# Kernel optimization log

Measured on AMD Instinct MI355X. Metric: run time of the kernel, lower is better.

The kernel has to match this reference:

```python
import jax, jax.numpy as jnp
import numpy as np

B, D1, SN, NF = 32, 49, 32, 16          # batch, n_sais, sqrt_n, n_filters
D_MODEL, HEADS = SN * SN * NF, 16        # 16384, 16
DEPTH = D_MODEL // HEADS                 # 1024
C_IN = 16


def setup_inputs() -> dict:
    key = jax.random.key(0)
    ks = jax.random.split(key, 11)
    mk = lambda k, shape, scale=1.0: jax.random.normal(k, shape, dtype=jnp.float32) * scale
    w_scale = 1.0 / np.sqrt(C_IN)
    return {
        "v": mk(ks[0], (B, D1, SN, SN, C_IN)),
        "k": mk(ks[1], (B, D1, SN, SN, C_IN)),
        "q": mk(ks[2], (B, D1, SN, SN, C_IN)),
        # 1x1x1 Conv3D == pointwise channel matmul: weight [C_in, n_filters] + bias
        "Wq": mk(ks[3], (C_IN, NF), w_scale), "bq": jnp.zeros((NF,), jnp.float32),
        "Wk": mk(ks[4], (C_IN, NF), w_scale), "bk": jnp.zeros((NF,), jnp.float32),
        "Wv": mk(ks[5], (C_IN, NF), w_scale), "bv": jnp.zeros((NF,), jnp.float32),
        "Wo": mk(ks[6], (NF, NF), w_scale),   "bo": jnp.zeros((NF,), jnp.float32),
    }


def _pointwise(x, W, b):
    # Conv3D(kernel=1, padding='same') over [B, d1, h, w, c]
    return jnp.einsum('bdhwc,cf->bdhwf', x, W) + b


def reference(v, k, q, Wq, bq, Wk, bk, Wv, bv, Wo, bo):
    b = q.shape[0]
    # projections (1x1x1 conv3d), then flatten spatial+channel into d_model
    def proj_heads(x, W, bias):
        y = _pointwise(x, W, bias).reshape(b, D1, D_MODEL)       # reshape2d
        y = y.reshape(b, D1, HEADS, DEPTH)                        # split_heads
        return y.transpose(0, 2, 1, 3)                            # [b, h, d1, depth]
    qh = proj_heads(q, Wq, bq)
    kh = proj_heads(k, Wk, bk)
    vh = proj_heads(v, Wv, bv)
    # scaled dot-product attention over the 49 SAI tokens
    scale = 1.0 / jnp.sqrt(jnp.float32(DEPTH))
    scores = jnp.einsum('bhqd,bhkd->bhqk', qh, kh) * scale        # [b, h, 49, 49]
    attn = jax.nn.softmax(scores, axis=-1)
    ctx = jnp.einsum('bhqk,bhkd->bhqd', attn, vh)                 # [b, h, 49, depth]
    ctx = ctx.transpose(0, 2, 1, 3).reshape(b, D1, D_MODEL)       # concat heads
    ctx = ctx.reshape(b, D1, SN, SN, NF)                          # reshape4d
    out = _pointwise(ctx, Wo, bo)                                 # wout conv3d 1x1x1
    return out, attn
```

## Files before the change

kernel.cpp:

```cpp
#include <hip/hip_runtime.h>
#include <hip/hip_bf16.h>


#define NT 49
#define TOKS 16384
#define HSL 1024
#define SLOT 3200
#define ZSWZ(n) (((((n) & 7) ^ (((n) >> 3) & 7))) << 4)

typedef __attribute__((ext_vector_type(8))) short bf16x8;
typedef __attribute__((ext_vector_type(4))) float f32x4;

__device__ __forceinline__ ushort f2bf(float f) {
    union { float f; unsigned u; } v; v.f = f;
    return (ushort)((v.u + 0x7fffu + ((v.u >> 16) & 1u)) >> 16);
}
__device__ __forceinline__ unsigned pk2(float lo, float hi) {
    return (unsigned)f2bf(lo) | ((unsigned)f2bf(hi) << 16);
}
__device__ __forceinline__ float qdot(f32x4 x0, f32x4 x1, f32x4 x2, f32x4 x3,
                                      f32x4 wa, f32x4 wb, f32x4 wc, f32x4 wd) {
    float s =      x0[0]*wa[0];
    s = fmaf(x0[1], wa[1], s); s = fmaf(x0[2], wa[2], s); s = fmaf(x0[3], wa[3], s);
    s = fmaf(x1[0], wb[0], s); s = fmaf(x1[1], wb[1], s); s = fmaf(x1[2], wb[2], s);
    s = fmaf(x1[3], wb[3], s);
    s = fmaf(x2[0], wc[0], s); s = fmaf(x2[1], wc[1], s); s = fmaf(x2[2], wc[2], s);
    s = fmaf(x2[3], wc[3], s);
    s = fmaf(x3[0], wd[0], s); s = fmaf(x3[1], wd[1], s); s = fmaf(x3[2], wd[2], s);
    s = fmaf(x3[3], wd[3], s);
    return s;
}

#define W_DECL(mb) \
    f32x4 W00 = *(const f32x4*)((mb)+ 0), W01 = *(const f32x4*)((mb)+ 4), \
          W02 = *(const f32x4*)((mb)+ 8), W03 = *(const f32x4*)((mb)+12), \
          W10 = *(const f32x4*)((mb)+16), W11 = *(const f32x4*)((mb)+20), \
          W12 = *(const f32x4*)((mb)+24), W13 = *(const f32x4*)((mb)+28), \
          W20 = *(const f32x4*)((mb)+32), W21 = *(const f32x4*)((mb)+36), \
          W22 = *(const f32x4*)((mb)+40), W23 = *(const f32x4*)((mb)+44), \
          W30 = *(const f32x4*)((mb)+48), W31 = *(const f32x4*)((mb)+52), \
          W32 = *(const f32x4*)((mb)+56), W33 = *(const f32x4*)((mb)+60)

__global__ __launch_bounds__(256, 2) void k_scores8(
    const float* __restrict__ qin, const float* __restrict__ kin,
    const float* __restrict__ Wq, const float* __restrict__ bq,
    const float* __restrict__ Wk, float* __restrict__ ws1)
{
    __shared__ ushort bufA[64*128];
    __shared__ ushort bufB[64*128];
    __shared__ float  Msh[256];
    __shared__ float  wkbqSh[16];
    __shared__ float  gSh[64];

    const int tid  = threadIdx.x;
    const int lane = tid & 63;
    const int wv   = tid >> 6;
    const int s    = blockIdx.x & 7;
    const int h    = (blockIdx.x >> 3) & 15;
    const int b    = blockIdx.x >> 7;

    const float* qbase = qin + (size_t)b*NT*TOKS + h*HSL + s*128;
    const float* kbase = kin + (size_t)b*NT*TOKS + h*HSL + s*128;

    const int f4 = tid & 31;
    const int t0 = tid >> 5;
    const int si = (tid >> 2) & 7;
    const int rq = tid & 3;

    f32x4 kv[7];
    {
        const float* kp = kbase + f4*4;
        #pragma unroll
        for (int i = 0; i < 7; ++i) {
            const int t = t0 + 8*i; const int tc = t < 48 ? t : 48;
            kv[i] = *(const f32x4*)(kp + (size_t)tc*TOKS);
        }
    }
    f32x4 q0[7], q1[7], q2[7], q3[7];
    {
        #pragma unroll
        for (int i = 0; i < 7; ++i) {
            const int t = t0 + 8*i; const int tc = t < 48 ? t : 48;
            const float* qc = qbase + si*16 + (size_t)tc*TOKS;
            q0[i] = *(const f32x4*)(qc);
            q1[i] = *(const f32x4*)(qc + 4);
            q2[i] = *(const f32x4*)(qc + 8);
            q3[i] = *(const f32x4*)(qc + 12);
        }
    }

    {
        unsigned* z0 = (unsigned*)bufA; unsigned* z1 = (unsigned*)bufB;
        #pragma unroll
        for (int i = 0; i < 16; ++i) { z0[tid + 256*i] = 0u; z1[tid + 256*i] = 0u; }
        const int c1 = tid >> 4, c2 = tid & 15;
        float m = 0.f;
        #pragma unroll
        for (int f = 0; f < 16; ++f) m += Wq[c1*16+f] * Wk[c2*16+f];
        Msh[c2*16 + c1] = m;
        if (tid < 16) {
            float wb = 0.f;
            #pragma unroll
            for (int g = 0; g < 16; ++g) wb += Wk[tid*16+g] * bq[g];
            wkbqSh[tid] = wb;
        }
        if (tid < 64) gSh[tid] = 0.f;
    }
    __syncthreads();

    W_DECL(Msh + rq*64);
    f32x4 wkb = *(const f32x4*)(wkbqSh + (f4 & 3)*4);

    #pragma unroll
    for (int i = 0; i < 7; ++i) {
        const int t = t0 + 8*i;
        f32x4 xk = kv[i];
        if (t >= NT) xk = (f32x4){0.f,0.f,0.f,0.f};
        uint2 w; w.x = pk2(xk[0], xk[1]); w.y = pk2(xk[2], xk[3]);
        *(uint2*)((char*)bufB + ((t*256 + f4*8) ^ ((t & 7) << 4))) = w;
        const float pg = xk[0]*wkb[0] + xk[1]*wkb[1] + xk[2]*wkb[2] + xk[3]*wkb[3];
        if (pg != 0.f) atomicAdd(&gSh[t], pg);
    }
    #pragma unroll
    for (int i = 0; i < 7; ++i) {
        const int t = t0 + 8*i;
        if (t < NT) {
            const float o0 = qdot(q0[i],q1[i],q2[i],q3[i], W00,W01,W02,W03);
            const float o1 = qdot(q0[i],q1[i],q2[i],q3[i], W10,W11,W12,W13);
            const float o2 = qdot(q0[i],q1[i],q2[i],q3[i], W20,W21,W22,W23);
            const float o3 = qdot(q0[i],q1[i],q2[i],q3[i], W30,W31,W32,W33);
            uint2 w; w.x = pk2(o0, o1); w.y = pk2(o2, o3);
            *(uint2*)((char*)bufA + ((t*256 + si*32 + rq*8) ^ ((t & 7) << 4))) = w;
        }
    }
    __syncthreads();

    f32x4 accS[4];
    #pragma unroll
    for (int nt = 0; nt < 4; ++nt) accS[nt] = (f32x4){0.f,0.f,0.f,0.f};
    #pragma unroll
    for (int ks = 0; ks < 4; ++ks) {
        const int ra  = wv*16 + (lane & 15);
        const int abo = (ra*256 + (ks*32 + (lane >> 4)*8)*2) ^ ((ra & 7) << 4);
        const bf16x8 af = *(const bf16x8*)((const char*)bufA + abo);
        #pragma unroll
        for (int nt = 0; nt < 4; ++nt) {
            const int rb  = nt*16 + (lane & 15);
            const int bbo = (rb*256 + (ks*32 + (lane >> 4)*8)*2) ^ ((rb & 7) << 4);
            const bf16x8 bf = *(const bf16x8*)((const char*)bufB + bbo);
            accS[nt] = __builtin_amdgcn_mfma_f32_16x16x32_bf16(af, bf, accS[nt], 0, 0, 0);
        }
    }

    float* slot = ws1 + (size_t)blockIdx.x * SLOT;
    #pragma unroll
    for (int nt = 0; nt < 4; ++nt) {
        const int col = nt*16 + (lane & 15);
        #pragma unroll
        for (int rr = 0; rr < 4; ++rr) {
            const int row = wv*16 + (lane >> 4)*4 + rr;
            if (row < NT) slot[row*64 + col] = accS[nt][rr];
        }
    }
    if (tid < 64) slot[3136 + tid] = gSh[tid];
}

template<int SPLIT, int LOG2S>
__global__ __launch_bounds__(256, 2) void k_scores(
    const float* __restrict__ qin, const float* __restrict__ kin,
    const float* __restrict__ Wq, const float* __restrict__ bq,
    const float* __restrict__ Wk, float* __restrict__ ws1)
{
    __shared__ ushort bufA[64*128];
    __shared__ ushort bufB[64*128];
    __shared__ float  Msh[256];
    __shared__ float  wkbqSh[16];
    __shared__ float  gSh[64];

    const int tid  = threadIdx.x;
    const int lane = tid & 63;
    const int wv   = tid >> 6;
    const int s    = blockIdx.x & (SPLIT - 1);
    const int h    = (blockIdx.x >> LOG2S) & 15;
    const int b    = blockIdx.x >> (LOG2S + 4);

    const float* qbase = qin + (size_t)b*NT*TOKS + h*HSL + s*(1024/SPLIT);
    const float* kbase = kin + (size_t)b*NT*TOKS + h*HSL + s*(1024/SPLIT);

    const int f4 = tid & 31;
    const int t0 = tid >> 5;
    const int si = (tid >> 2) & 7;
    const int rq = tid & 3;

    constexpr int NC = 8 / SPLIT;

    f32x4 kv[7];
    {
        const float* kp = kbase + f4*4;
        #pragma unroll
        for (int i = 0; i < 7; ++i) {
            const int t = t0 + 8*i; const int tc = t < 48 ? t : 48;
            kv[i] = *(const f32x4*)(kp + (size_t)tc*TOKS);
        }
    }
    f32x4 xa0, xa1, xa2, xa3;
    {
        const float* qc = qbase + si*16 + (size_t)t0*TOKS;
        xa0 = *(const f32x4*)(qc);
        xa1 = *(const f32x4*)(qc + 4);
        xa2 = *(const f32x4*)(qc + 8);
        xa3 = *(const f32x4*)(qc + 12);
    }

    {
        unsigned* z0 = (unsigned*)bufA; unsigned* z1 = (unsigned*)bufB;
        #pragma unroll
        for (int i = 0; i < 16; ++i) { z0[tid + 256*i] = 0u; z1[tid + 256*i] = 0u; }
        const int c1 = tid >> 4, c2 = tid & 15;
        float m = 0.f;
        #pragma unroll
        for (int f = 0; f < 16; ++f) m += Wq[c1*16+f] * Wk[c2*16+f];
        Msh[c2*16 + c1] = m;
        if (tid < 16) {
            float wb = 0.f;
            #pragma unroll
            for (int g = 0; g < 16; ++g) wb += Wk[tid*16+g] * bq[g];
            wkbqSh[tid] = wb;
        }
        if (tid < 64) gSh[tid] = 0.f;
    }
    __syncthreads();

    W_DECL(Msh + rq*64);
    f32x4 wkb = *(const f32x4*)(wkbqSh + (f4 & 3)*4);

    f32x4 accS[4];
    #pragma unroll
    for (int nt = 0; nt < 4; ++nt) accS[nt] = (f32x4){0.f,0.f,0.f,0.f};

    for (int kc = 0; kc < NC; ++kc) {
        if (kc > 0) {
            const float* kp = kbase + kc*128 + f4*4;
            #pragma unroll
            for (int i = 0; i < 7; ++i) {
                const int t = t0 + 8*i; const int tc = t < 48 ? t : 48;
                kv[i] = *(const f32x4*)(kp + (size_t)tc*TOKS);
            }
            const float* qc = qbase + kc*128 + si*16 + (size_t)t0*TOKS;
            xa0 = *(const f32x4*)(qc);
            xa1 = *(const f32x4*)(qc + 4);
            xa2 = *(const f32x4*)(qc + 8);
            xa3 = *(const f32x4*)(qc + 12);
        }
        #pragma unroll
        for (int i = 0; i < 7; ++i) {
            const int t = t0 + 8*i;
            f32x4 xk = kv[i];
            if (t >= NT) xk = (f32x4){0.f,0.f,0.f,0.f};
            uint2 w; w.x = pk2(xk[0], xk[1]); w.y = pk2(xk[2], xk[3]);
            *(uint2*)((char*)bufB + ((t*256 + f4*8) ^ ((t & 7) << 4))) = w;
            const float pg = xk[0]*wkb[0] + xk[1]*wkb[1] + xk[2]*wkb[2] + xk[3]*wkb[3];
            if (pg != 0.f) atomicAdd(&gSh[t], pg);
        }
        #pragma unroll
        for (int i = 0; i < 7; ++i) {
            f32x4 xb0 = xa0, xb1 = xa1, xb2 = xa2, xb3 = xa3;
            if (i < 6) {
                const int tn = t0 + 8*(i+1); const int tc = tn < 48 ? tn : 48;
                const float* qc = qbase + kc*128 + si*16 + (size_t)tc*TOKS;
                xb0 = *(const f32x4*)(qc);
                xb1 = *(const f32x4*)(qc + 4);
                xb2 = *(const f32x4*)(qc + 8);
                xb3 = *(const f32x4*)(qc + 12);
            }
            const int t = t0 + 8*i;
            if (t < NT) {
                const float o0 = qdot(xa0,xa1,xa2,xa3, W00,W01,W02,W03);
                const float o1 = qdot(xa0,xa1,xa2,xa3, W10,W11,W12,W13);
                const float o2 = qdot(xa0,xa1,xa2,xa3, W20,W21,W22,W23);
                const float o3 = qdot(xa0,xa1,xa2,xa3, W30,W31,W32,W33);
                uint2 w; w.x = pk2(o0, o1); w.y = pk2(o2, o3);
                *(uint2*)((char*)bufA + ((t*256 + si*32 + rq*8) ^ ((t & 7) << 4))) = w;
            }
            xa0 = xb0; xa1 = xb1; xa2 = xb2; xa3 = xb3;
        }
        __syncthreads();
        #pragma unroll
        for (int ks = 0; ks < 4; ++ks) {
            const int ra  = wv*16 + (lane & 15);
            const int abo = (ra*256 + (ks*32 + (lane >> 4)*8)*2) ^ ((ra & 7) << 4);
            const bf16x8 af = *(const bf16x8*)((const char*)bufA + abo);
            #pragma unroll
            for (int nt = 0; nt < 4; ++nt) {
                const int rb  = nt*16 + (lane & 15);
                const int bbo = (rb*256 + (ks*32 + (lane >> 4)*8)*2) ^ ((rb & 7) << 4);
                const bf16x8 bf = *(const bf16x8*)((const char*)bufB + bbo);
                accS[nt] = __builtin_amdgcn_mfma_f32_16x16x32_bf16(af, bf, accS[nt], 0, 0, 0);
            }
        }
        if (kc + 1 < NC) __syncthreads();
    }

    float* slot = ws1 + (size_t)blockIdx.x * SLOT;
    #pragma unroll
    for (int nt = 0; nt < 4; ++nt) {
        const int col = nt*16 + (lane & 15);
        #pragma unroll
        for (int rr = 0; rr < 4; ++rr) {
            const int row = wv*16 + (lane >> 4)*4 + rr;
            if (row < NT) slot[row*64 + col] = accS[nt][rr];
        }
    }
    if (tid < 64) slot[3136 + tid] = gSh[tid];
}

template<int SPLIT>
__global__ __launch_bounds__(256, 2) void k_softmax(
    const float* __restrict__ ws1, float* __restrict__ attnp,
    ushort* __restrict__ ws2)
{
    __shared__ float sS[NT*69];
    __shared__ float sG[64];
    const int tid = threadIdx.x;
    const float* base = ws1 + (size_t)blockIdx.x * SPLIT * SLOT;

    for (int p = tid; p < 784; p += 256) {
        const int row = p >> 4, c4 = (p & 15) * 4;
        float4 acc = *(const float4*)(base + row*64 + c4);
        #pragma unroll
        for (int s = 1; s < SPLIT; ++s) {
            const float4 a = *(const float4*)(base + s*SLOT + row*64 + c4);
            acc.x += a.x; acc.y += a.y; acc.z += a.z; acc.w += a.w;
        }
        sS[row*69 + c4 + 0] = acc.x;
        sS[row*69 + c4 + 1] = acc.y;
        sS[row*69 + c4 + 2] = acc.z;
        sS[row*69 + c4 + 3] = acc.w;
    }
    if (tid < 64) {
        float g = base[3136 + tid];
        #pragma unroll
        for (int s = 1; s < SPLIT; ++s) g += base[s*SLOT + 3136 + tid];
        sG[tid] = g;
    }
    __syncthreads();

    if (tid < NT) {
        float mx = -1e30f;
        for (int j = 0; j < NT; ++j) {
            const float v = (sS[tid*69 + j] + sG[j]) * 0.03125f;
            sS[tid*69 + j] = v;
            mx = fmaxf(mx, v);
        }
        float ssum = 0.f;
        for (int j = 0; j < NT; ++j) {
            const float e = __expf(sS[tid*69 + j] - mx);
            sS[tid*69 + j] = e; ssum += e;
        }
        const float inv = 1.0f / ssum;
        for (int j = 0; j < NT; ++j) sS[tid*69 + j] *= inv;
    }
    __syncthreads();

    float* ab = attnp + (size_t)blockIdx.x * (NT*NT);
    for (int p = tid; p < NT*NT; p += 256) {
        const int t = p / NT, j = p - t*NT;
        ab[p] = sS[t*69 + j];
    }
    ushort* w2 = ws2 + (size_t)blockIdx.x * 4096;
    for (int p = tid; p < 4096; p += 256) {
        const int t = p >> 6, j = p & 63;
        const float v = (t < NT && j < NT) ? sS[t*69 + j] : 0.f;
        w2[p] = f2bf(v);
    }
}

__global__ __launch_bounds__(256, 2) void k_out(
    const float* __restrict__ vin,
    const float* __restrict__ Wv, const float* __restrict__ bv,
    const float* __restrict__ Wo, const float* __restrict__ bo,
    const ushort* __restrict__ ws2, float* __restrict__ out)
{
    __shared__ unsigned Zt[4096];
    __shared__ float WvoSh[256];
    __shared__ float bvoSh[16];

    const int tid  = threadIdx.x;
    const int lane = tid & 63;
    const int wv   = tid >> 6;
    const int kc   = blockIdx.x & 7;
    const int h    = (blockIdx.x >> 3) & 15;
    const int b    = blockIdx.x >> 7;
    const float* vbase = vin + (size_t)b*NT*TOKS + h*HSL;

    const int si = (tid >> 2) & 7;
    const int rq = tid & 3;
    const int t0 = tid >> 5;

    const ushort* w2 = ws2 + ((size_t)(blockIdx.x >> 3)) * 4096;
    const int ra = wv*16 + (lane & 15);
    const bf16x8 af0 = *(const bf16x8*)(w2 + ra*64 +      (lane >> 4)*8);
    const bf16x8 af1 = *(const bf16x8*)(w2 + ra*64 + 32 + (lane >> 4)*8);
    f32x4 xa0, xa1, xa2, xa3;
    {
        const float* vc = vbase + kc*128 + si*16 + (size_t)t0*TOKS;
        xa0 = *(const f32x4*)(vc);
        xa1 = *(const f32x4*)(vc + 4);
        xa2 = *(const f32x4*)(vc + 8);
        xa3 = *(const f32x4*)(vc + 12);
    }

    {
        const int c1 = tid >> 4, c2 = tid & 15;
        float wvo = 0.f;
        #pragma unroll
        for (int f = 0; f < 16; ++f) wvo += Wv[c1*16+f] * Wo[f*16+c2];
        WvoSh[c2*16 + c1] = wvo;
        if (tid < 16) {
            float s2 = 0.f;
            #pragma unroll
            for (int g = 0; g < 16; ++g) s2 += bv[g]*Wo[g*16+tid];
            bvoSh[tid] = s2 + bo[tid];
        }
        #pragma unroll
        for (int i = 0; i < 16; ++i) Zt[tid + 256*i] = 0u;
    }
    __syncthreads();

    W_DECL(WvoSh + rq*64);
    const float bias = bvoSh[lane & 15];

    #pragma unroll
    for (int i = 0; i < 7; ++i) {
        f32x4 xb0 = xa0, xb1 = xa1, xb2 = xa2, xb3 = xa3;
        if (i < 6) {
            const int tn = t0 + 8*(i+1); const int tc = tn < 48 ? tn : 48;
            const float* vc = vbase + kc*128 + si*16 + (size_t)tc*TOKS;
            xb0 = *(const f32x4*)(vc);
            xb1 = *(const f32x4*)(vc + 4);
            xb2 = *(const f32x4*)(vc + 8);
            xb3 = *(const f32x4*)(vc + 12);
        }
        const int t = t0 + 8*i;
        if (t < NT) {
            const float o0 = qdot(xa0,xa1,xa2,xa3, W00,W01,W02,W03);
            const float o1 = qdot(xa0,xa1,xa2,xa3, W10,W11,W12,W13);
            const float o2 = qdot(xa0,xa1,xa2,xa3, W20,W21,W22,W23);
            const float o3 = qdot(xa0,xa1,xa2,xa3, W30,W31,W32,W33);
            const int n0 = si*16 + rq*4;
            const int pb = (t >> 1)*4, hb = (t & 1)*2;
            *(ushort*)((char*)Zt + ((((n0+0)*128 + pb) ^ ZSWZ(n0+0)) + hb)) = f2bf(o0);
            *(ushort*)((char*)Zt + ((((n0+1)*128 + pb) ^ ZSWZ(n0+1)) + hb)) = f2bf(o1);
            *(ushort*)((char*)Zt + ((((n0+2)*128 + pb) ^ ZSWZ(n0+2)) + hb)) = f2bf(o2);
            *(ushort*)((char*)Zt + ((((n0+3)*128 + pb) ^ ZSWZ(n0+3)) + hb)) = f2bf(o3);
        }
        xa0 = xb0; xa1 = xb1; xa2 = xb2; xa3 = xb3;
    }
    __syncthreads();

    float* obase = out + (size_t)b*NT*TOKS + h*HSL + kc*128;
    #pragma unroll
    for (int nt2 = 0; nt2 < 8; ++nt2) {
        const int n    = nt2*16 + (lane & 15);
        const int swzn = ZSWZ(n);
        const bf16x8 bf0 = *(const bf16x8*)((const char*)Zt + ((n*128 +      (lane >> 4)*16) ^ swzn));
        const bf16x8 bf1 = *(const bf16x8*)((const char*)Zt + ((n*128 + 64 + (lane >> 4)*16) ^ swzn));
        f32x4 acc = (f32x4){0.f, 0.f, 0.f, 0.f};
        acc = __builtin_amdgcn_mfma_f32_16x16x32_bf16(af0, bf0, acc, 0, 0, 0);
        acc = __builtin_amdgcn_mfma_f32_16x16x32_bf16(af1, bf1, acc, 0, 0, 0);
        #pragma unroll
        for (int r2 = 0; r2 < 4; ++r2) {
            const int row = wv*16 + (lane >> 4)*4 + r2;
            if (row < NT) obase[(size_t)row*TOKS + n] = acc[r2] + bias;
        }
    }
}

extern "C" void kernel_launch(void* const* d_in, const int* in_sizes, int n_in,
                              void* d_out, int out_size, void* d_ws, size_t ws_size,
                              hipStream_t stream) {
    const float* v  = (const float*)d_in[0];
    const float* k  = (const float*)d_in[1];
    const float* q  = (const float*)d_in[2];
    const float* Wq = (const float*)d_in[3];
    const float* bq = (const float*)d_in[4];
    const float* Wk = (const float*)d_in[5];
    const float* bk = (const float*)d_in[6];
    const float* Wv = (const float*)d_in[7];
    const float* bv = (const float*)d_in[8];
    const float* Wo = (const float*)d_in[9];
    const float* bo = (const float*)d_in[10];
    (void)bk; (void)in_sizes; (void)n_in; (void)out_size;

    float* outp  = (float*)d_out;
    float* attnp = outp + (size_t)32 * 49 * 16384;
    float* ws1   = (float*)d_ws;

    const size_t need8 = (size_t)4096*SLOT*4 + (size_t)512*4096*2;
    const size_t need4 = (size_t)2048*SLOT*4 + (size_t)512*4096*2;
    if (ws_size >= need8) {
        ushort* ws2 = (ushort*)(ws1 + (size_t)4096*SLOT);
        k_scores8    <<<dim3(4096), dim3(256), 0, stream>>>(q, k, Wq, bq, Wk, ws1);
        k_softmax<8> <<<dim3(512),  dim3(256), 0, stream>>>(ws1, attnp, ws2);
        k_out        <<<dim3(4096), dim3(256), 0, stream>>>(v, Wv, bv, Wo, bo, ws2, outp);
    } else if (ws_size >= need4) {
        ushort* ws2 = (ushort*)(ws1 + (size_t)2048*SLOT);
        k_scores<4,2><<<dim3(2048), dim3(256), 0, stream>>>(q, k, Wq, bq, Wk, ws1);
        k_softmax<4> <<<dim3(512),  dim3(256), 0, stream>>>(ws1, attnp, ws2);
        k_out        <<<dim3(4096), dim3(256), 0, stream>>>(v, Wv, bv, Wo, bo, ws2, outp);
    } else {
        ushort* ws2 = (ushort*)(ws1 + (size_t)1024*SLOT);
        k_scores<2,1><<<dim3(1024), dim3(256), 0, stream>>>(q, k, Wq, bq, Wk, ws1);
        k_softmax<2> <<<dim3(512),  dim3(256), 0, stream>>>(ws1, attnp, ws2);
        k_out        <<<dim3(4096), dim3(256), 0, stream>>>(v, Wv, bv, Wo, bo, ws2, outp);
    }
}
```

Before: 129.9 us.

## Halve scores LDS tiles via two-pass K staging and preload all V rows

```diff
diff --git a/kernel.cpp b/kernel.cpp
--- a/kernel.cpp
+++ b/kernel.cpp
@@ -7,6 +7,7 @@
 #define HSL 1024
 #define SLOT 3200
 #define ZSWZ(n) (((((n) & 7) ^ (((n) >> 3) & 7))) << 4)
+#define SW64(t) (((t) & 7) << 4)
 
 typedef __attribute__((ext_vector_type(8))) short bf16x8;
 typedef __attribute__((ext_vector_type(4))) float f32x4;
@@ -46,8 +47,8 @@
     const float* __restrict__ Wq, const float* __restrict__ bq,
     const float* __restrict__ Wk, float* __restrict__ ws1)
 {
-    __shared__ ushort bufA[64*128];
-    __shared__ ushort bufB[64*128];
+    __shared__ ushort bufA[64*64];
+    __shared__ ushort bufB[64*64];
     __shared__ float  Msh[256];
     __shared__ float  wkbqSh[16];
     __shared__ float  gSh[64];
@@ -77,22 +78,23 @@
         }
     }
     f32x4 q0[7], q1[7], q2[7], q3[7];
+    #pragma unroll
+    for (int i = 0; i < 7; ++i) {
+        const int t = t0 + 8*i; const int tc = t < 48 ? t : 48;
+        const float* qc = qbase + si*16 + (size_t)tc*TOKS;
+        q0[i] = *(const f32x4*)(qc);
+        q1[i] = *(const f32x4*)(qc + 4);
+        q2[i] = *(const f32x4*)(qc + 8);
+        q3[i] = *(const f32x4*)(qc + 12);
+    }
+
     {
-        #pragma unroll
-        for (int i = 0; i < 7; ++i) {
-            const int t = t0 + 8*i; const int tc = t < 48 ? t : 48;
-            const float* qc = qbase + si*16 + (size_t)tc*TOKS;
-            q0[i] = *(const f32x4*)(qc);
-            q1[i] = *(const f32x4*)(qc + 4);
-            q2[i] = *(const f32x4*)(qc + 8);
-            q3[i] = *(const f32x4*)(qc + 12);
-        }
-    }
-
-    {
-        unsigned* z0 = (unsigned*)bufA; unsigned* z1 = (unsigned*)bufB;
-        #pragma unroll
-        for (int i = 0; i < 16; ++i) { z0[tid + 256*i] = 0u; z1[tid + 256*i] = 0u; }
+        unsigned* zA = (unsigned*)bufA; unsigned* zB = (unsigned*)bufB;
+        #pragma unroll
+        for (int i = 0; i < 2; ++i) {
+            const int j = tid + 256*i;
+            if (j < 480) { zA[1568 + j] = 0u; zB[1568 + j] = 0u; }
+        }
         const int c1 = tid >> 4, c2 = tid & 15;
         float m = 0.f;
         #pragma unroll
@@ -109,47 +111,67 @@
     __syncthreads();
 
     W_DECL(Msh + rq*64);
-    f32x4 wkb = *(const f32x4*)(wkbqSh + (f4 & 3)*4);
-
+    const f32x4 wkb = *(const f32x4*)(wkbqSh + (f4 & 3)*4);
+
+    uint2 kw[7];
     #pragma unroll
     for (int i = 0; i < 7; ++i) {
         const int t = t0 + 8*i;
         f32x4 xk = kv[i];
         if (t >= NT) xk = (f32x4){0.f,0.f,0.f,0.f};
-        uint2 w; w.x = pk2(xk[0], xk[1]); w.y = pk2(xk[2], xk[3]);
-        *(uint2*)((char*)bufB + ((t*256 + f4*8) ^ ((t & 7) << 4))) = w;
+        kw[i].x = pk2(xk[0], xk[1]); kw[i].y = pk2(xk[2], xk[3]);
         const float pg = xk[0]*wkb[0] + xk[1]*wkb[1] + xk[2]*wkb[2] + xk[3]*wkb[3];
         if (pg != 0.f) atomicAdd(&gSh[t], pg);
     }
+    uint2 qw[7];
     #pragma unroll
     for (int i = 0; i < 7; ++i) {
-        const int t = t0 + 8*i;
-        if (t < NT) {
-            const float o0 = qdot(q0[i],q1[i],q2[i],q3[i], W00,W01,W02,W03);
-            const float o1 = qdot(q0[i],q1[i],q2[i],q3[i], W10,W11,W12,W13);
-            const float o2 = qdot(q0[i],q1[i],q2[i],q3[i], W20,W21,W22,W23);
-            const float o3 = qdot(q0[i],q1[i],q2[i],q3[i], W30,W31,W32,W33);
-            uint2 w; w.x = pk2(o0, o1); w.y = pk2(o2, o3);
-            *(uint2*)((char*)bufA + ((t*256 + si*32 + rq*8) ^ ((t & 7) << 4))) = w;
-        }
-    }
-    __syncthreads();
+        const float o0 = qdot(q0[i],q1[i],q2[i],q3[i], W00,W01,W02,W03);
+        const float o1 = qdot(q0[i],q1[i],q2[i],q3[i], W10,W11,W12,W13);
+        const float o2 = qdot(q0[i],q1[i],q2[i],q3[i], W20,W21,W22,W23);
+        const float o3 = qdot(q0[i],q1[i],q2[i],q3[i], W30,W31,W32,W33);
+        qw[i].x = pk2(o0, o1); qw[i].y = pk2(o2, o3);
+    }
+
+    const int f4h = f4 >> 4, f4l = f4 & 15;
+    const int sih = si >> 2, sil = si & 3;
+    const int ra  = wv*16 + (lane & 15);
 
     f32x4 accS[4];
     #pragma unroll
     for (int nt = 0; nt < 4; ++nt) accS[nt] = (f32x4){0.f,0.f,0.f,0.f};
-    #pragma unroll
-    for (int ks = 0; ks < 4; ++ks) {
-        const int ra  = wv*16 + (lane & 15);
-        const int abo = (ra*256 + (ks*32 + (lane >> 4)*8)*2) ^ ((ra & 7) << 4);
-        const bf16x8 af = *(const bf16x8*)((const char*)bufA + abo);
-        #pragma unroll
-        for (int nt = 0; nt < 4; ++nt) {
-            const int rb  = nt*16 + (lane & 15);
-            const int bbo = (rb*256 + (ks*32 + (lane >> 4)*8)*2) ^ ((rb & 7) << 4);
-            const bf16x8 bf = *(const bf16x8*)((const char*)bufB + bbo);
-            accS[nt] = __builtin_amdgcn_mfma_f32_16x16x32_bf16(af, bf, accS[nt], 0, 0, 0);
-        }
+
+    #pragma unroll
+    for (int h2 = 0; h2 < 2; ++h2) {
+        if (f4h == h2) {
+            #pragma unroll
+            for (int i = 0; i < 7; ++i) {
+                const int t = t0 + 8*i;
+                *(uint2*)((char*)bufB + ((t*128 + f4l*8) ^ SW64(t))) = kw[i];
+            }
+        }
+        if (sih == h2) {
+            #pragma unroll
+            for (int i = 0; i < 7; ++i) {
+                const int t = t0 + 8*i;
+                if (t < NT)
+                    *(uint2*)((char*)bufA + ((t*128 + sil*32 + rq*8) ^ SW64(t))) = qw[i];
+            }
+        }
+        __syncthreads();
+        #pragma unroll
+        for (int ks2 = 0; ks2 < 2; ++ks2) {
+            const int abo = (ra*128 + ks2*64 + (lane >> 4)*16) ^ SW64(ra);
+            const bf16x8 af = *(const bf16x8*)((const char*)bufA + abo);
+            #pragma unroll
+            for (int nt = 0; nt < 4; ++nt) {
+                const int rb  = nt*16 + (lane & 15);
+                const int bbo = (rb*128 + ks2*64 + (lane >> 4)*16) ^ SW64(rb);
+                const bf16x8 bf = *(const bf16x8*)((const char*)bufB + bbo);
+                accS[nt] = __builtin_amdgcn_mfma_f32_16x16x32_bf16(af, bf, accS[nt], 0, 0, 0);
+            }
+        }
+        if (h2 == 0) __syncthreads();
     }
 
     float* slot = ws1 + (size_t)blockIdx.x * SLOT;
@@ -401,13 +423,15 @@
     const int ra = wv*16 + (lane & 15);
     const bf16x8 af0 = *(const bf16x8*)(w2 + ra*64 +      (lane >> 4)*8);
     const bf16x8 af1 = *(const bf16x8*)(w2 + ra*64 + 32 + (lane >> 4)*8);
-    f32x4 xa0, xa1, xa2, xa3;
-    {
-        const float* vc = vbase + kc*128 + si*16 + (size_t)t0*TOKS;
-        xa0 = *(const f32x4*)(vc);
-        xa1 = *(const f32x4*)(vc + 4);
-        xa2 = *(const f32x4*)(vc + 8);
-        xa3 = *(const f32x4*)(vc + 12);
+    f32x4 v0[7], v1[7], v2[7], v3[7];
+    #pragma unroll
+    for (int i = 0; i < 7; ++i) {
+        const int t = t0 + 8*i; const int tc = t < 48 ? t : 48;
+        const float* vc = vbase + kc*128 + si*16 + (size_t)tc*TOKS;
+        v0[i] = *(const f32x4*)(vc);
+        v1[i] = *(const f32x4*)(vc + 4);
+        v2[i] = *(const f32x4*)(vc + 8);
+        v3[i] = *(const f32x4*)(vc + 12);
     }
 
     {
@@ -432,21 +456,12 @@
 
     #pragma unroll
     for (int i = 0; i < 7; ++i) {
-        f32x4 xb0 = xa0, xb1 = xa1, xb2 = xa2, xb3 = xa3;
-        if (i < 6) {
-            const int tn = t0 + 8*(i+1); const int tc = tn < 48 ? tn : 48;
-            const float* vc = vbase + kc*128 + si*16 + (size_t)tc*TOKS;
-            xb0 = *(const f32x4*)(vc);
-            xb1 = *(const f32x4*)(vc + 4);
-            xb2 = *(const f32x4*)(vc + 8);
-            xb3 = *(const f32x4*)(vc + 12);
-        }
         const int t = t0 + 8*i;
         if (t < NT) {
-            const float o0 = qdot(xa0,xa1,xa2,xa3, W00,W01,W02,W03);
-            const float o1 = qdot(xa0,xa1,xa2,xa3, W10,W11,W12,W13);
-            const float o2 = qdot(xa0,xa1,xa2,xa3, W20,W21,W22,W23);
-            const float o3 = qdot(xa0,xa1,xa2,xa3, W30,W31,W32,W33);
+            const float o0 = qdot(v0[i],v1[i],v2[i],v3[i], W00,W01,W02,W03);
+            const float o1 = qdot(v0[i],v1[i],v2[i],v3[i], W10,W11,W12,W13);
+            const float o2 = qdot(v0[i],v1[i],v2[i],v3[i], W20,W21,W22,W23);
+            const float o3 = qdot(v0[i],v1[i],v2[i],v3[i], W30,W31,W32,W33);
             const int n0 = si*16 + rq*4;
             const int pb = (t >> 1)*4, hb = (t & 1)*2;
             *(ushort*)((char*)Zt + ((((n0+0)*128 + pb) ^ ZSWZ(n0+0)) + hb)) = f2bf(o0);
@@ -454,7 +469,6 @@
             *(ushort*)((char*)Zt + ((((n0+2)*128 + pb) ^ ZSWZ(n0+2)) + hb)) = f2bf(o2);
             *(ushort*)((char*)Zt + ((((n0+3)*128 + pb) ^ ZSWZ(n0+3)) + hb)) = f2bf(o3);
         }
-        xa0 = xb0; xa1 = xb1; xa2 = xb2; xa3 = xb3;
     }
     __syncthreads();
 
```

Result: slower. 138.9 us (+7.0%).
